# Kernel optimization log

Measured on AMD Instinct MI355X. Metric: run time of the kernel, lower is better.

Reference implementation:

```python
import jax, jax.numpy as jnp
import numpy as np
import math

N_HEAD = 16
D_MODEL = 1024
KSIZE = 3
PAD = 1


def _conv1d(x, w, b, pad):
    # x: [B, C_in, S], w: [C_out, C_in, K] (torch Conv1d layout)
    y = jax.lax.conv_general_dilated(
        x, w, window_strides=(1,), padding=[(pad, pad)],
        dimension_numbers=("NCH", "OIH", "NCH"))
    return y + b[None, :, None]


def setup_inputs() -> dict:
    key = jax.random.key(0)
    ks = jax.random.split(key, 10)
    B, S, D = 2, 2048, D_MODEL
    sc = 1.0 / math.sqrt(D)
    return {
        "q": jax.random.normal(ks[0], (B, S, D), jnp.float32),
        "k": jax.random.normal(ks[1], (B, S, D), jnp.float32),
        "v": jax.random.normal(ks[2], (B, S, D), jnp.float32),
        "wq_w": jax.random.normal(ks[3], (D, D, KSIZE), jnp.float32) * sc,
        "wq_b": jnp.zeros((D,), jnp.float32),
        "wk_w": jax.random.normal(ks[4], (D, D, KSIZE), jnp.float32) * sc,
        "wk_b": jnp.zeros((D,), jnp.float32),
        "wv_w": jax.random.normal(ks[5], (D, D, 1), jnp.float32) * sc,
        "wv_b": jnp.zeros((D,), jnp.float32),
        "wc_w": jax.random.normal(ks[6], (D, D), jnp.float32) * sc,
        "wc_b": jnp.zeros((D,), jnp.float32),
    }


def reference(q, k, v, wq_w, wq_b, wk_w, wk_b, wv_w, wv_b, wc_w, wc_b):
    B, S, D = q.shape
    h = N_HEAD
    d = D // h
    # channels-first for conv projections: [B, D, S]
    qc = _conv1d(jnp.swapaxes(q, 1, 2), wq_w, wq_b, PAD)
    kc = _conv1d(jnp.swapaxes(k, 1, 2), wk_w, wk_b, PAD)
    vc = _conv1d(jnp.swapaxes(v, 1, 2), wv_w, wv_b, 0)
    # faithful to torch: view(b, d, h, s) then transpose(1,2).transpose(2,3) -> [b, h, s, d]
    # (head index is the FAST axis of the channel dim, matching the original)
    qh = jnp.transpose(qc.reshape(B, d, h, S), (0, 2, 3, 1))
    kh = jnp.transpose(kc.reshape(B, d, h, S), (0, 2, 3, 1))
    vh = jnp.transpose(vc.reshape(B, d, h, S), (0, 2, 3, 1))
    scores = jnp.einsum("bhqd,bhkd->bhqk", qh, kh) / math.sqrt(d)
    attn = jax.nn.softmax(scores, axis=-1)
    out = jnp.einsum("bhqk,bhkd->bhqd", attn, vh)
    # concat: [b,h,s,d] -> [b,s,h*d]
    out = jnp.transpose(out, (0, 2, 1, 3)).reshape(B, S, D)
    # torch Linear: x @ W^T + b
    return out @ wc_w.T + wc_b
```

## Files before the change

### kernel.cpp

```cpp
#include <hip/hip_runtime.h>
#include <hip/hip_bf16.h>

#define SS 2048
#define DDIM 1024

typedef unsigned short u16;
typedef unsigned int u32;
typedef __attribute__((ext_vector_type(8))) short bf16x8_t;
typedef __attribute__((ext_vector_type(4))) float f32x4_t;

__device__ __forceinline__ u16 f2bf(float f) {
  __hip_bfloat16 h = __float2bfloat16(f);
  return *reinterpret_cast<u16*>(&h);
}

__device__ __forceinline__ void gld16(const void* g, void* lds_base) {
  __builtin_amdgcn_global_load_lds(
      (const __attribute__((address_space(1))) u32*)(uintptr_t)g,
      (__attribute__((address_space(3))) u32*)(u32)(uintptr_t)lds_base,
      16, 0, 0);
}

__global__ void zero_kernel(u32* zb) { zb[threadIdx.x] = 0u; }

__global__ __launch_bounds__(256) void convert3_kernel(
    const float* __restrict__ q, const float* __restrict__ k,
    const float* __restrict__ v, u16* __restrict__ Xq, u16* __restrict__ Xk,
    u16* __restrict__ Xv) {
  const int z = blockIdx.y;
  const float* src = (z == 0) ? q : (z == 1) ? k : v;
  u16* dst = (z == 0) ? Xq : (z == 1) ? Xk : Xv;
  int i = blockIdx.x * 256 + threadIdx.x;
  const float4* s = (const float4*)src + (size_t)i * 2;
  float4 f0 = s[0], f1 = s[1];
  u16 o[8] = {f2bf(f0.x), f2bf(f0.y), f2bf(f0.z), f2bf(f0.w),
              f2bf(f1.x), f2bf(f1.y), f2bf(f1.z), f2bf(f1.w)};
  *(uint4*)(dst + (size_t)i * 8) = *(const uint4*)o;
}

__global__ __launch_bounds__(256) void repack3_kernel(
    const float* __restrict__ wq, const float* __restrict__ wk,
    u16* __restrict__ Wqr, u16* __restrict__ Wkr) {
  const float* w = blockIdx.y ? wk : wq;
  u16* out = blockIdx.y ? Wkr : Wqr;
  int o = blockIdx.x;
  for (int j = threadIdx.x; j < 3072; j += 256) {
    int i = j / 3, t = j - i * 3;
    out[(size_t)o * 3072 + t * 1024 + i] = f2bf(w[(size_t)o * 3072 + j]);
  }
}

__global__ __launch_bounds__(256) void repackc_kernel(
    const float* __restrict__ wv, const float* __restrict__ wc,
    u16* __restrict__ Wvr, u16* __restrict__ Wcr) {
  const float* w = blockIdx.y ? wc : wv;
  u16* out = blockIdx.y ? Wcr : Wvr;
  size_t i = (size_t)blockIdx.x * 1024 + threadIdx.x * 4;
  float4 f = *(const float4*)(w + i);
  u16 o4[4] = {f2bf(f.x), f2bf(f.y), f2bf(f.z), f2bf(f.w)};
  *(ushort4*)(out + i) = *(const ushort4*)o4;
}

__global__ __launch_bounds__(256) void mfma_proj(
    const u16* __restrict__ Xq, const u16* __restrict__ Xk,
    const u16* __restrict__ Xv, const u16* __restrict__ Wq,
    const u16* __restrict__ Wk, const u16* __restrict__ Wv,
    const float* __restrict__ bq, const float* __restrict__ bk,
    const float* __restrict__ bv, u16* __restrict__ Qhb,
    u16* __restrict__ Khb, u16* __restrict__ Vtb,
    const u16* __restrict__ zbuf) {
  __shared__ __attribute__((aligned(16))) u16 As[128][40];
  __shared__ __attribute__((aligned(16))) u16 Bs[128][40];
  const int z = blockIdx.z;
  const u16* __restrict__ Xb = (z == 0) ? Xq : (z == 1) ? Xk : Xv;
  const u16* __restrict__ Wr = (z == 0) ? Wq : (z == 1) ? Wk : Wv;
  const float* __restrict__ bias = (z == 0) ? bq : (z == 1) ? bk : bv;
  u16* __restrict__ Cptr = (z == 0) ? Qhb : (z == 1) ? Khb : Vtb;
  const int Kdim = (z == 2) ? 1024 : 3072;
  const bool conv = (z < 2);
  const bool vout = (z == 2);
  const float scale = (z == 0) ? 0.125f : 1.0f;

  const int tid = threadIdx.x;
  const int lane = tid & 63;
  const int w = tid >> 6;
  const int ln = tid & 15;
  const int quad = (tid >> 4) & 3;
  const int wrow = w >> 1, wcol = w & 1;
  const int m0 = blockIdx.x * 128, n0 = blockIdx.y * 128;

  f32x4_t acc[4][4];
#pragma unroll
  for (int i = 0; i < 4; ++i)
#pragma unroll
    for (int j = 0; j < 4; ++j) acc[i][j] = (f32x4_t){0.f, 0.f, 0.f, 0.f};

  for (int k0 = 0; k0 < Kdim; k0 += 32) {
    __syncthreads();
    for (int c = w; c < 10; c += 4) {
      int G = c * 64 + lane;
      int x = G / 5, kb = G - x * 5;
      if (kb < 4) {
        int gm = m0 + x;
        const u16* src;
        if (conv) {
          int b = gm >> 11, s = gm & 2047;
          int t = k0 >> 10;
          int sp = s + t - 1;
          src = (sp >= 0 && sp < SS)
                    ? Xb + ((size_t)(b * SS + sp) * DDIM + (k0 & 1023) + kb * 8)
                    : zbuf;
        } else {
          src = Xb + ((size_t)gm * DDIM + k0 + kb * 8);
        }
        gld16(src, (char*)As + c * 1024);
      }
    }
    for (int c = w; c < 10; c += 4) {
      int G = c * 64 + lane;
      int x = G / 5, kb = G - x * 5;
      if (kb < 4) {
        const u16* src = Wr + (size_t)(n0 + x) * Kdim + k0 + kb * 8;
        gld16(src, (char*)Bs + c * 1024);
      }
    }
    __syncthreads();

    bf16x8_t a[4], b[4];
#pragma unroll
    for (int mt = 0; mt < 4; ++mt)
      a[mt] = *(const bf16x8_t*)&As[wrow * 64 + mt * 16 + ln][quad * 8];
#pragma unroll
    for (int nt = 0; nt < 4; ++nt)
      b[nt] = *(const bf16x8_t*)&Bs[wcol * 64 + nt * 16 + ln][quad * 8];
#pragma unroll
    for (int mt = 0; mt < 4; ++mt)
#pragma unroll
      for (int nt = 0; nt < 4; ++nt)
        acc[mt][nt] = __builtin_amdgcn_mfma_f32_16x16x32_bf16(
            a[mt], b[nt], acc[mt][nt], 0, 0, 0);
  }

#pragma unroll
  for (int mt = 0; mt < 4; ++mt) {
#pragma unroll
    for (int nt = 0; nt < 4; ++nt) {
      int gn = n0 + wcol * 64 + nt * 16 + ln;
      float bi = bias[gn];
#pragma unroll
      for (int r = 0; r < 4; ++r) {
        int gm = m0 + wrow * 64 + mt * 16 + quad * 4 + r;
        float val = (acc[mt][nt][r] + bi) * scale;
        int b = gm >> 11, s = gm & 2047;
        int hh = gn & 15, dd = gn >> 4;
        if (!vout)
          Cptr[((size_t)(b * 16 + hh) * SS + s) * 64 + dd] = f2bf(val);
        else
          Cptr[((size_t)(b * 16 + hh) * 64 + dd) * SS + s] = f2bf(val);
      }
    }
  }
}

__global__ __launch_bounds__(256) void mfma_gemm_lin(
    const u16* __restrict__ Xb, const u16* __restrict__ Wr,
    const float* __restrict__ bias, float* __restrict__ Cptr) {
  __shared__ __attribute__((aligned(16))) u16 As[128][40];
  __shared__ __attribute__((aligned(16))) u16 Bs[128][40];
  const int tid = threadIdx.x;
  const int lane = tid & 63;
  const int w = tid >> 6;
  const int ln = tid & 15;
  const int quad = (tid >> 4) & 3;
  const int wrow = w >> 1, wcol = w & 1;
  const int m0 = blockIdx.x * 128, n0 = blockIdx.y * 128;

  f32x4_t acc[4][4];
#pragma unroll
  for (int i = 0; i < 4; ++i)
#pragma unroll
    for (int j = 0; j < 4; ++j) acc[i][j] = (f32x4_t){0.f, 0.f, 0.f, 0.f};

  for (int k0 = 0; k0 < 1024; k0 += 32) {
    __syncthreads();
    for (int c = w; c < 10; c += 4) {
      int G = c * 64 + lane;
      int x = G / 5, kb = G - x * 5;
      if (kb < 4)
        gld16(Xb + ((size_t)(m0 + x) * DDIM + k0 + kb * 8), (char*)As + c * 1024);
    }
    for (int c = w; c < 10; c += 4) {
      int G = c * 64 + lane;
      int x = G / 5, kb = G - x * 5;
      if (kb < 4)
        gld16(Wr + (size_t)(n0 + x) * 1024 + k0 + kb * 8, (char*)Bs + c * 1024);
    }
    __syncthreads();

    bf16x8_t a[4], b[4];
#pragma unroll
    for (int mt = 0; mt < 4; ++mt)
      a[mt] = *(const bf16x8_t*)&As[wrow * 64 + mt * 16 + ln][quad * 8];
#pragma unroll
    for (int nt = 0; nt < 4; ++nt)
      b[nt] = *(const bf16x8_t*)&Bs[wcol * 64 + nt * 16 + ln][quad * 8];
#pragma unroll
    for (int mt = 0; mt < 4; ++mt)
#pragma unroll
      for (int nt = 0; nt < 4; ++nt)
        acc[mt][nt] = __builtin_amdgcn_mfma_f32_16x16x32_bf16(
            a[mt], b[nt], acc[mt][nt], 0, 0, 0);
  }

#pragma unroll
  for (int mt = 0; mt < 4; ++mt) {
#pragma unroll
    for (int nt = 0; nt < 4; ++nt) {
      int gn = n0 + wcol * 64 + nt * 16 + ln;
      float bi = bias[gn];
#pragma unroll
      for (int r = 0; r < 4; ++r) {
        int gm = m0 + wrow * 64 + mt * 16 + quad * 4 + r;
        Cptr[(size_t)gm * DDIM + gn] = acc[mt][nt][r] + bi;
      }
    }
  }
}

__global__ __launch_bounds__(256) void mfma_attn(
    const u16* __restrict__ Qhb, const u16* __restrict__ Khb,
    const u16* __restrict__ Vtb, u16* __restrict__ Aob,
    const u16* __restrict__ zbuf) {
  __shared__ __attribute__((aligned(16))) u16 Ks[64][72];
  __shared__ __attribute__((aligned(16))) u16 Vt[64][72];
  __shared__ __attribute__((aligned(16))) u16 Ps[4][16][72];
  const int tid = threadIdx.x;
  const int lane = tid & 63;
  const int w = tid >> 6;
  const int ln = tid & 15;
  const int quad = (tid >> 4) & 3;
  const int bh = blockIdx.y;
  const int b = bh >> 4, hh = bh & 15;
  const int s0 = blockIdx.x * 64;

  const u16* qp = Qhb + ((size_t)bh * SS + s0 + w * 16 + ln) * 64 + quad * 8;
  bf16x8_t qf0 = *(const bf16x8_t*)qp;
  bf16x8_t qf1 = *(const bf16x8_t*)(qp + 32);

  float mrow[4], lsum[4];
  f32x4_t oacc[4];
#pragma unroll
  for (int r = 0; r < 4; ++r) { mrow[r] = -3e38f; lsum[r] = 0.f; }
#pragma unroll
  for (int dt = 0; dt < 4; ++dt) oacc[dt] = (f32x4_t){0.f, 0.f, 0.f, 0.f};

  for (int kt = 0; kt < 32; ++kt) {
    __syncthreads();
    for (int c = w; c < 9; c += 4) {
      int G = c * 64 + lane;
      int x = G / 9, db = G - x * 9;
      if (db < 8) {
        gld16(Khb + ((size_t)bh * SS + kt * 64 + x) * 64 + db * 8,
              (char*)Ks + c * 1024);
        gld16(Vtb + ((size_t)bh * 64 + x) * SS + kt * 64 + db * 8,
              (char*)Vt + c * 1024);
      }
    }
    __syncthreads();

    f32x4_t sc[4];
#pragma unroll
    for (int nt = 0; nt < 4; ++nt) sc[nt] = (f32x4_t){0.f, 0.f, 0.f, 0.f};
#pragma unroll
    for (int nt = 0; nt < 4; ++nt) {
      bf16x8_t k0f = *(const bf16x8_t*)&Ks[nt * 16 + ln][quad * 8];
      sc[nt] = __builtin_amdgcn_mfma_f32_16x16x32_bf16(qf0, k0f, sc[nt], 0, 0, 0);
      bf16x8_t k1f = *(const bf16x8_t*)&Ks[nt * 16 + ln][32 + quad * 8];
      sc[nt] = __builtin_amdgcn_mfma_f32_16x16x32_bf16(qf1, k1f, sc[nt], 0, 0, 0);
    }

    float mxv[4];
    bool need = false;
#pragma unroll
    for (int r = 0; r < 4; ++r) {
      float mx = fmaxf(fmaxf(sc[0][r], sc[1][r]), fmaxf(sc[2][r], sc[3][r]));
      mx = fmaxf(mx, __shfl_xor(mx, 1, 64));
      mx = fmaxf(mx, __shfl_xor(mx, 2, 64));
      mx = fmaxf(mx, __shfl_xor(mx, 4, 64));
      mx = fmaxf(mx, __shfl_xor(mx, 8, 64));
      mxv[r] = mx;
      need = need || (mx > mrow[r]);
    }
    if (__any(need)) {
#pragma unroll
      for (int r = 0; r < 4; ++r) {
        float mn = fmaxf(mrow[r], mxv[r]);
        float al = __expf(mrow[r] - mn);
        mrow[r] = mn;
        lsum[r] *= al;
#pragma unroll
        for (int dt = 0; dt < 4; ++dt) oacc[dt][r] *= al;
      }
    }
#pragma unroll
    for (int r = 0; r < 4; ++r) {
      float p0 = __expf(sc[0][r] - mrow[r]), p1 = __expf(sc[1][r] - mrow[r]);
      float p2 = __expf(sc[2][r] - mrow[r]), p3 = __expf(sc[3][r] - mrow[r]);
      lsum[r] += p0 + p1 + p2 + p3;
      Ps[w][quad * 4 + r][ln] = f2bf(p0);
      Ps[w][quad * 4 + r][16 + ln] = f2bf(p1);
      Ps[w][quad * 4 + r][32 + ln] = f2bf(p2);
      Ps[w][quad * 4 + r][48 + ln] = f2bf(p3);
    }

    bf16x8_t pa0 = *(const bf16x8_t*)&Ps[w][ln][quad * 8];
    bf16x8_t pa1 = *(const bf16x8_t*)&Ps[w][ln][32 + quad * 8];
#pragma unroll
    for (int dt = 0; dt < 4; ++dt) {
      bf16x8_t v0f = *(const bf16x8_t*)&Vt[dt * 16 + ln][quad * 8];
      oacc[dt] = __builtin_amdgcn_mfma_f32_16x16x32_bf16(pa0, v0f, oacc[dt], 0, 0, 0);
      bf16x8_t v1f = *(const bf16x8_t*)&Vt[dt * 16 + ln][32 + quad * 8];
      oacc[dt] = __builtin_amdgcn_mfma_f32_16x16x32_bf16(pa1, v1f, oacc[dt], 0, 0, 0);
    }
  }

  float inv[4];
#pragma unroll
  for (int r = 0; r < 4; ++r) {
    float t = lsum[r];
    t += __shfl_xor(t, 1, 64);
    t += __shfl_xor(t, 2, 64);
    t += __shfl_xor(t, 4, 64);
    t += __shfl_xor(t, 8, 64);
    inv[r] = 1.f / t;
  }
#pragma unroll
  for (int dt = 0; dt < 4; ++dt)
#pragma unroll
    for (int r = 0; r < 4; ++r) {
      int gm = b * SS + s0 + w * 16 + quad * 4 + r;
      Aob[(size_t)gm * DDIM + hh * 64 + dt * 16 + ln] = f2bf(oacc[dt][r] * inv[r]);
    }
}

extern "C" void kernel_launch(void* const* d_in, const int* in_sizes, int n_in,
                              void* d_out, int out_size, void* d_ws, size_t ws_size,
                              hipStream_t stream) {
  const float* q    = (const float*)d_in[0];
  const float* k    = (const float*)d_in[1];
  const float* v    = (const float*)d_in[2];
  const float* wq_w = (const float*)d_in[3];
  const float* wq_b = (const float*)d_in[4];
  const float* wk_w = (const float*)d_in[5];
  const float* wk_b = (const float*)d_in[6];
  const float* wv_w = (const float*)d_in[7];
  const float* wv_b = (const float*)d_in[8];
  const float* wc_w = (const float*)d_in[9];
  const float* wc_b = (const float*)d_in[10];

  char* ws = (char*)d_ws;
  size_t off = 0;
  u16* zbuf = (u16*)(ws + off); off += 256;
  const size_t SZ_ACT = (size_t)2 * SS * DDIM * 2;
  u16* Xq  = (u16*)(ws + off); off += SZ_ACT;
  u16* Xk  = (u16*)(ws + off); off += SZ_ACT;
  u16* Xv  = (u16*)(ws + off); off += SZ_ACT;
  u16* Wqr = (u16*)(ws + off); off += (size_t)1024 * 3072 * 2;
  u16* Wkr = (u16*)(ws + off); off += (size_t)1024 * 3072 * 2;
  u16* Wvr = (u16*)(ws + off); off += (size_t)1024 * 1024 * 2;
  u16* Wcr = (u16*)(ws + off); off += (size_t)1024 * 1024 * 2;
  u16* Qhb = (u16*)(ws + off); off += SZ_ACT;
  u16* Khb = (u16*)(ws + off); off += SZ_ACT;
  u16* Vtb = (u16*)(ws + off); off += SZ_ACT;
  u16* Aob = (u16*)(ws + off); off += SZ_ACT;
  if (ws_size < off) return;

  zero_kernel<<<1, 64, 0, stream>>>((u32*)zbuf);
  convert3_kernel<<<dim3(2048, 3), 256, 0, stream>>>(q, k, v, Xq, Xk, Xv);
  repack3_kernel<<<dim3(1024, 2), 256, 0, stream>>>(wq_w, wk_w, Wqr, Wkr);
  repackc_kernel<<<dim3(1024, 2), 256, 0, stream>>>(wv_w, wc_w, Wvr, Wcr);

  mfma_proj<<<dim3(32, 8, 3), 256, 0, stream>>>(
      Xq, Xk, Xv, Wqr, Wkr, Wvr, wq_b, wk_b, wv_b, Qhb, Khb, Vtb, zbuf);

  mfma_attn<<<dim3(32, 32), 256, 0, stream>>>(Qhb, Khb, Vtb, Aob, zbuf);

  mfma_gemm_lin<<<dim3(32, 8), 256, 0, stream>>>(Aob, Wcr, wc_b, (float*)d_out);
}
```

Measured before the change: 436.9 us.

## Double-buffer LDS tiles in projection, attention and output GEMM; shrink output tile rows

The projection GEMM, the attention kernel and the output linear GEMM now use two LDS buffers. The next K-step (or K/V tile) is issued with global_load_lds before the MFMA work on the current buffer, which removes one barrier per iteration and overlaps global loads with compute. The output linear GEMM also moves from 128x128 to 32x128 tiles, launching 4x more blocks to fill the CUs. In exchange, LDS use doubles per block, which may lower occupancy, and the smaller output tiles reuse each loaded weight tile less.

```diff
diff --git a/kernel.cpp b/kernel.cpp
--- a/kernel.cpp
+++ b/kernel.cpp
@@ -69,17 +69,18 @@
     const float* __restrict__ bv, u16* __restrict__ Qhb,
     u16* __restrict__ Khb, u16* __restrict__ Vtb,
     const u16* __restrict__ zbuf) {
-  __shared__ __attribute__((aligned(16))) u16 As[128][40];
-  __shared__ __attribute__((aligned(16))) u16 Bs[128][40];
+  __shared__ __attribute__((aligned(16))) u16 As2[2][128][40];
+  __shared__ __attribute__((aligned(16))) u16 Bs2[2][128][40];
   const int z = blockIdx.z;
   const u16* __restrict__ Xb = (z == 0) ? Xq : (z == 1) ? Xk : Xv;
   const u16* __restrict__ Wr = (z == 0) ? Wq : (z == 1) ? Wk : Wv;
   const float* __restrict__ bias = (z == 0) ? bq : (z == 1) ? bk : bv;
   u16* __restrict__ Cptr = (z == 0) ? Qhb : (z == 1) ? Khb : Vtb;
-  const int Kdim = (z == 2) ? 1024 : 3072;
+  const int nk = (z == 2) ? 32 : 96;
   const bool conv = (z < 2);
   const bool vout = (z == 2);
   const float scale = (z == 0) ? 0.125f : 1.0f;
+  const int Kdim = (z == 2) ? 1024 : 3072;
 
   const int tid = threadIdx.x;
   const int lane = tid & 63;
@@ -89,14 +90,8 @@
   const int wrow = w >> 1, wcol = w & 1;
   const int m0 = blockIdx.x * 128, n0 = blockIdx.y * 128;
 
-  f32x4_t acc[4][4];
-#pragma unroll
-  for (int i = 0; i < 4; ++i)
-#pragma unroll
-    for (int j = 0; j < 4; ++j) acc[i][j] = (f32x4_t){0.f, 0.f, 0.f, 0.f};
-
-  for (int k0 = 0; k0 < Kdim; k0 += 32) {
-    __syncthreads();
+  auto stage = [&](int ks, int bi) {
+    int k0 = ks * 32;
     for (int c = w; c < 10; c += 4) {
       int G = c * 64 + lane;
       int x = G / 5, kb = G - x * 5;
@@ -113,19 +108,33 @@
         } else {
           src = Xb + ((size_t)gm * DDIM + k0 + kb * 8);
         }
-        gld16(src, (char*)As + c * 1024);
+        gld16(src, (char*)As2[bi] + c * 1024);
       }
     }
     for (int c = w; c < 10; c += 4) {
       int G = c * 64 + lane;
       int x = G / 5, kb = G - x * 5;
-      if (kb < 4) {
-        const u16* src = Wr + (size_t)(n0 + x) * Kdim + k0 + kb * 8;
-        gld16(src, (char*)Bs + c * 1024);
-      }
-    }
-    __syncthreads();
-
+      if (kb < 4)
+        gld16(Wr + (size_t)(n0 + x) * Kdim + k0 + kb * 8,
+              (char*)Bs2[bi] + c * 1024);
+    }
+  };
+
+  f32x4_t acc[4][4];
+#pragma unroll
+  for (int i = 0; i < 4; ++i)
+#pragma unroll
+    for (int j = 0; j < 4; ++j) acc[i][j] = (f32x4_t){0.f, 0.f, 0.f, 0.f};
+
+  stage(0, 0);
+  __syncthreads();
+
+  for (int ks = 0; ks < nk; ++ks) {
+    int cur = ks & 1;
+    if (ks + 1 < nk) stage(ks + 1, cur ^ 1);
+
+    const u16(*As)[40] = As2[cur];
+    const u16(*Bs)[40] = Bs2[cur];
     bf16x8_t a[4], b[4];
 #pragma unroll
     for (int mt = 0; mt < 4; ++mt)
@@ -139,6 +148,8 @@
       for (int nt = 0; nt < 4; ++nt)
         acc[mt][nt] = __builtin_amdgcn_mfma_f32_16x16x32_bf16(
             a[mt], b[nt], acc[mt][nt], 0, 0, 0);
+
+    __syncthreads();
   }
 
 #pragma unroll
@@ -165,64 +176,67 @@
 __global__ __launch_bounds__(256) void mfma_gemm_lin(
     const u16* __restrict__ Xb, const u16* __restrict__ Wr,
     const float* __restrict__ bias, float* __restrict__ Cptr) {
-  __shared__ __attribute__((aligned(16))) u16 As[128][40];
-  __shared__ __attribute__((aligned(16))) u16 Bs[128][40];
+  __shared__ __attribute__((aligned(16))) u16 As2[2][32][40];
+  __shared__ __attribute__((aligned(16))) u16 Bs2[2][128][40];
   const int tid = threadIdx.x;
   const int lane = tid & 63;
   const int w = tid >> 6;
   const int ln = tid & 15;
   const int quad = (tid >> 4) & 3;
   const int wrow = w >> 1, wcol = w & 1;
-  const int m0 = blockIdx.x * 128, n0 = blockIdx.y * 128;
-
-  f32x4_t acc[4][4];
-#pragma unroll
-  for (int i = 0; i < 4; ++i)
-#pragma unroll
-    for (int j = 0; j < 4; ++j) acc[i][j] = (f32x4_t){0.f, 0.f, 0.f, 0.f};
-
-  for (int k0 = 0; k0 < 1024; k0 += 32) {
-    __syncthreads();
+  const int m0 = blockIdx.x * 32, n0 = blockIdx.y * 128;
+
+  auto stage = [&](int ks, int bi) {
+    int k0 = ks * 32;
+    for (int c = w; c < 3; c += 4) {
+      int G = c * 64 + lane;
+      int x = G / 5, kb = G - x * 5;
+      if (kb < 4 && x < 32)
+        gld16(Xb + ((size_t)(m0 + x) * DDIM + k0 + kb * 8),
+              (char*)As2[bi] + c * 1024);
+    }
     for (int c = w; c < 10; c += 4) {
       int G = c * 64 + lane;
       int x = G / 5, kb = G - x * 5;
       if (kb < 4)
-        gld16(Xb + ((size_t)(m0 + x) * DDIM + k0 + kb * 8), (char*)As + c * 1024);
-    }
-    for (int c = w; c < 10; c += 4) {
-      int G = c * 64 + lane;
-      int x = G / 5, kb = G - x * 5;
-      if (kb < 4)
-        gld16(Wr + (size_t)(n0 + x) * 1024 + k0 + kb * 8, (char*)Bs + c * 1024);
-    }
-    __syncthreads();
-
-    bf16x8_t a[4], b[4];
-#pragma unroll
-    for (int mt = 0; mt < 4; ++mt)
-      a[mt] = *(const bf16x8_t*)&As[wrow * 64 + mt * 16 + ln][quad * 8];
+        gld16(Wr + (size_t)(n0 + x) * 1024 + k0 + kb * 8,
+              (char*)Bs2[bi] + c * 1024);
+    }
+  };
+
+  f32x4_t acc[4];
+#pragma unroll
+  for (int j = 0; j < 4; ++j) acc[j] = (f32x4_t){0.f, 0.f, 0.f, 0.f};
+
+  stage(0, 0);
+  __syncthreads();
+
+  for (int ks = 0; ks < 32; ++ks) {
+    int cur = ks & 1;
+    if (ks + 1 < 32) stage(ks + 1, cur ^ 1);
+
+    const u16(*As)[40] = As2[cur];
+    const u16(*Bs)[40] = Bs2[cur];
+    bf16x8_t a = *(const bf16x8_t*)&As[wrow * 16 + ln][quad * 8];
+    bf16x8_t b[4];
 #pragma unroll
     for (int nt = 0; nt < 4; ++nt)
       b[nt] = *(const bf16x8_t*)&Bs[wcol * 64 + nt * 16 + ln][quad * 8];
 #pragma unroll
-    for (int mt = 0; mt < 4; ++mt)
-#pragma unroll
-      for (int nt = 0; nt < 4; ++nt)
-        acc[mt][nt] = __builtin_amdgcn_mfma_f32_16x16x32_bf16(
-            a[mt], b[nt], acc[mt][nt], 0, 0, 0);
-  }
-
-#pragma unroll
-  for (int mt = 0; mt < 4; ++mt) {
-#pragma unroll
-    for (int nt = 0; nt < 4; ++nt) {
-      int gn = n0 + wcol * 64 + nt * 16 + ln;
-      float bi = bias[gn];
-#pragma unroll
-      for (int r = 0; r < 4; ++r) {
-        int gm = m0 + wrow * 64 + mt * 16 + quad * 4 + r;
-        Cptr[(size_t)gm * DDIM + gn] = acc[mt][nt][r] + bi;
-      }
+    for (int nt = 0; nt < 4; ++nt)
+      acc[nt] = __builtin_amdgcn_mfma_f32_16x16x32_bf16(a, b[nt], acc[nt], 0, 0, 0);
+
+    __syncthreads();
+  }
+
+#pragma unroll
+  for (int nt = 0; nt < 4; ++nt) {
+    int gn = n0 + wcol * 64 + nt * 16 + ln;
+    float bi = bias[gn];
+#pragma unroll
+    for (int r = 0; r < 4; ++r) {
+      int gm = m0 + wrow * 16 + quad * 4 + r;
+      Cptr[(size_t)gm * DDIM + gn] = acc[nt][r] + bi;
     }
   }
 }
@@ -231,8 +245,8 @@
     const u16* __restrict__ Qhb, const u16* __restrict__ Khb,
     const u16* __restrict__ Vtb, u16* __restrict__ Aob,
     const u16* __restrict__ zbuf) {
-  __shared__ __attribute__((aligned(16))) u16 Ks[64][72];
-  __shared__ __attribute__((aligned(16))) u16 Vt[64][72];
+  __shared__ __attribute__((aligned(16))) u16 Ks2[2][64][72];
+  __shared__ __attribute__((aligned(16))) u16 Vt2[2][64][72];
   __shared__ __attribute__((aligned(16))) u16 Ps[4][16][72];
   const int tid = threadIdx.x;
   const int lane = tid & 63;
@@ -243,30 +257,39 @@
   const int b = bh >> 4, hh = bh & 15;
   const int s0 = blockIdx.x * 64;
 
-  const u16* qp = Qhb + ((size_t)bh * SS + s0 + w * 16 + ln) * 64 + quad * 8;
-  bf16x8_t qf0 = *(const bf16x8_t*)qp;
-  bf16x8_t qf1 = *(const bf16x8_t*)(qp + 32);
-
-  float mrow[4], lsum[4];
-  f32x4_t oacc[4];
-#pragma unroll
-  for (int r = 0; r < 4; ++r) { mrow[r] = -3e38f; lsum[r] = 0.f; }
-#pragma unroll
-  for (int dt = 0; dt < 4; ++dt) oacc[dt] = (f32x4_t){0.f, 0.f, 0.f, 0.f};
-
-  for (int kt = 0; kt < 32; ++kt) {
-    __syncthreads();
+  auto stage = [&](int kt, int bi) {
     for (int c = w; c < 9; c += 4) {
       int G = c * 64 + lane;
       int x = G / 9, db = G - x * 9;
       if (db < 8) {
         gld16(Khb + ((size_t)bh * SS + kt * 64 + x) * 64 + db * 8,
-              (char*)Ks + c * 1024);
+              (char*)Ks2[bi] + c * 1024);
         gld16(Vtb + ((size_t)bh * 64 + x) * SS + kt * 64 + db * 8,
-              (char*)Vt + c * 1024);
+              (char*)Vt2[bi] + c * 1024);
       }
     }
-    __syncthreads();
+  };
+
+  const u16* qp = Qhb + ((size_t)bh * SS + s0 + w * 16 + ln) * 64 + quad * 8;
+  bf16x8_t qf0 = *(const bf16x8_t*)qp;
+  bf16x8_t qf1 = *(const bf16x8_t*)(qp + 32);
+
+  float mrow[4], lsum[4];
+  f32x4_t oacc[4];
+#pragma unroll
+  for (int r = 0; r < 4; ++r) { mrow[r] = -3e38f; lsum[r] = 0.f; }
+#pragma unroll
+  for (int dt = 0; dt < 4; ++dt) oacc[dt] = (f32x4_t){0.f, 0.f, 0.f, 0.f};
+
+  stage(0, 0);
+  __syncthreads();
+
+  for (int kt = 0; kt < 32; ++kt) {
+    int cur = kt & 1;
+    if (kt + 1 < 32) stage(kt + 1, cur ^ 1);
+
+    const u16(*Ks)[72] = Ks2[cur];
+    const u16(*Vt)[72] = Vt2[cur];
 
     f32x4_t sc[4];
 #pragma unroll
@@ -322,6 +345,8 @@
       bf16x8_t v1f = *(const bf16x8_t*)&Vt[dt * 16 + ln][32 + quad * 8];
       oacc[dt] = __builtin_amdgcn_mfma_f32_16x16x32_bf16(pa1, v1f, oacc[dt], 0, 0, 0);
     }
+
+    __syncthreads();
   }
 
   float inv[4];
@@ -385,5 +410,5 @@
 
   mfma_attn<<<dim3(32, 32), 256, 0, stream>>>(Qhb, Khb, Vtb, Aob, zbuf);
 
-  mfma_gemm_lin<<<dim3(32, 8), 256, 0, stream>>>(Aob, Wcr, wc_b, (float*)d_out);
-}
+  mfma_gemm_lin<<<dim3(128, 8), 256, 0, stream>>>(Aob, Wcr, wc_b, (float*)d_out);
+}
```

Measured after the change: 441.3 us. About the same (+1.0%).
